# Kernel optimization log

Measured on AMD Instinct MI355X. Metric: run time of the kernel, lower is better.

Reference implementation:

```python
import jax, jax.numpy as jnp
import numpy as np

NUM_ENT = 50000
N = 4 * NUM_ENT          # concat of id/gender/age/level embeds along dim 0
D = 128                  # init_dim = gcn_dim = embed_dim
H = 4                    # k_kernel attention heads
E = 600000
NUM_REL = 10
B = 4096


def _seg_softmax(scores, seg, n):
    # scores: [E, H], softmax over edges sharing the same destination node
    m = jax.ops.segment_max(scores, seg, num_segments=n)
    m = jnp.where(jnp.isfinite(m), m, 0.0)
    e = jnp.exp(scores - m[seg])
    s = jax.ops.segment_sum(e, seg, num_segments=n)
    return e / (s[seg] + 1e-16)


def _rgat_conv(x, rel_emb, src, dst, edge_type, W, W_rel, att):
    # CompGCN-style relational message (x_src + r_et) @ W, GAT-style attention,
    # per-destination segment softmax, scatter-sum aggregate, tanh activation.
    n = x.shape[0]
    xW = x @ W                        # [N, D_out]
    rW = rel_emb @ W                  # relation embed in message space
    d_out = xW.shape[1]
    dh = d_out // H
    m = (xW[src] + rW[edge_type]).reshape(-1, H, dh)   # [E, H, dh] messages
    q = xW[dst].reshape(-1, H, dh)                     # [E, H, dh] dest feats
    score = jax.nn.leaky_relu(
        (q * att[:, :dh]).sum(-1) + (m * att[:, dh:]).sum(-1), 0.2)  # [E, H]
    alpha = _seg_softmax(score, dst, n)                # [E, H]
    out = jax.ops.segment_sum((alpha[..., None] * m).reshape(-1, d_out), dst,
                              num_segments=n)          # [N, D_out]
    return jnp.tanh(out), rel_emb @ W_rel


def setup_inputs() -> dict:
    key = jax.random.key(0)
    ks = jax.random.split(key, 16)
    s = 0.1  # weight scale for numerical sanity
    return {
        "sub": jax.random.randint(ks[0], (B,), 0, N),
        "rel": jax.random.randint(ks[1], (B,), 0, 2 * NUM_REL),
        "edge_index": jax.random.randint(ks[2], (2, E), 0, N),
        "edge_type": jax.random.randint(ks[3], (E,), 0, 2 * NUM_REL),
        "ent_feature": jax.random.randint(ks[4], (NUM_ENT, 3), 0, 8),
        "gender_weight": s * jax.random.normal(ks[5], (8, D), jnp.float32),
        "age_weight": s * jax.random.normal(ks[6], (8, D), jnp.float32),
        "level_weight": s * jax.random.normal(ks[7], (8, D), jnp.float32),
        "id_embed": s * jax.random.normal(ks[8], (NUM_ENT, D), jnp.float32),
        "init_rel": s * jax.random.normal(ks[9], (2 * NUM_REL, D), jnp.float32),
        "W1": s * jax.random.normal(ks[10], (D, D), jnp.float32),
        "Wr1": s * jax.random.normal(ks[11], (D, D), jnp.float32),
        "att1": s * jax.random.normal(ks[12], (H, 2 * (D // H)), jnp.float32),
        "W2": s * jax.random.normal(ks[13], (D, D), jnp.float32),
        "Wr2": s * jax.random.normal(ks[14], (D, D), jnp.float32),
        "att2": s * jax.random.normal(ks[15], (H, 2 * (D // H)), jnp.float32),
    }


def reference(sub, rel, edge_index, edge_type, ent_feature,
              gender_weight, age_weight, level_weight, id_embed, init_rel,
              W1, Wr1, att1, W2, Wr2, att2):
    # feature embedding gathers + concat along node axis (as in __init__)
    gender_embed = gender_weight[ent_feature[:, 0]]
    age_embed = age_weight[ent_feature[:, 1]]
    level_embed = level_weight[ent_feature[:, 2]]
    x = jnp.concatenate([id_embed, gender_embed, age_embed, level_embed], axis=0)  # [N, D]
    src, dst = edge_index[0], edge_index[1]
    r = init_rel
    x, r = _rgat_conv(x, r, src, dst, edge_type, W1, Wr1, att1)
    # dropout modules run as identity (eval mode)
    x, r = _rgat_conv(x, r, src, dst, edge_type, W2, Wr2, att2)
    sub_emb = x[sub]
    rel_emb = r[rel]
    return (sub_emb, rel_emb, x)
```

## Files before the change

kernel.cpp:

```cpp
#include <hip/hip_runtime.h>

#define D 128
#define HEADS 4

typedef __attribute__((ext_vector_type(8))) short short8;
typedef __attribute__((ext_vector_type(4))) float f32x4;

__device__ __forceinline__ short f2b(float f) {
    unsigned u = __float_as_uint(f);
    unsigned r = (u + 0x7FFFu + ((u >> 16) & 1u)) >> 16;
    return (short)r;
}

__global__ __launch_bounds__(256) void gemm_mfma(
    const unsigned short* __restrict__ Ab, const short* __restrict__ Wt,
    unsigned short* __restrict__ C, const float* __restrict__ att,
    float* __restrict__ ns, int buildmode,
    const int* __restrict__ ent_feature, const float* __restrict__ gw,
    const float* __restrict__ aw, const float* __restrict__ lw,
    const float* __restrict__ idemb, int num_ent)
{
    __shared__ short sA[64 * D];
    __shared__ short sW[D * D];

    const int t = threadIdx.x;
    const long row0 = (long)blockIdx.x * 64;

    {
        int srow = t >> 2;
        int q = t & 3;
        long grow = row0 + srow;
        if (buildmode == 2) {
            const short8* p8 = (const short8*)(Ab + grow * D);
            #pragma unroll
            for (int jb = 0; jb < 4; ++jb) {
                short8 blk = p8[q * 4 + jb];
                int kb = (q * 4 + jb) ^ (srow & 7);
                *(short8*)&sA[srow * D + kb * 8] = blk;
            }
        } else {
            const float* srcp;
            if (grow < num_ent)               srcp = idemb + grow * D;
            else if (grow < 2L * num_ent)     srcp = gw + (long)ent_feature[(grow - num_ent) * 3 + 0] * D;
            else if (grow < 3L * num_ent)     srcp = aw + (long)ent_feature[(grow - 2L * num_ent) * 3 + 1] * D;
            else                              srcp = lw + (long)ent_feature[(grow - 3L * num_ent) * 3 + 2] * D;
            const float4* p4 = (const float4*)srcp + q * 8;
            float v[32];
            #pragma unroll
            for (int j = 0; j < 8; ++j) {
                float4 f = p4[j];
                v[j * 4 + 0] = f.x; v[j * 4 + 1] = f.y; v[j * 4 + 2] = f.z; v[j * 4 + 3] = f.w;
            }
            #pragma unroll
            for (int jb = 0; jb < 4; ++jb) {
                short8 blk;
                #pragma unroll
                for (int e = 0; e < 8; ++e) blk[e] = f2b(v[jb * 8 + e]);
                int kb = (q * 4 + jb) ^ (srow & 7);
                *(short8*)&sA[srow * D + kb * 8] = blk;
            }
        }
    }

    {
        #pragma unroll
        for (int i = 0; i < 8; ++i) {
            int c = t + 256 * i;
            int row = c >> 4, kb = c & 15;
            short8 blk = *(const short8*)(Wt + c * 8);
            *(short8*)&sW[row * D + (kb ^ (row & 7)) * 8] = blk;
        }
    }
    __syncthreads();

    const int wv = t >> 6, lane = t & 63;
    const int cl = lane & 15, kg = lane >> 4;

    short8 a[4];
    #pragma unroll
    for (int ks = 0; ks < 4; ++ks)
        a[ks] = *(const short8*)&sA[(wv * 16 + cl) * D + (((ks * 4 + kg) ^ (cl & 7)) * 8)];

    f32x4 acc[8];
    #pragma unroll
    for (int ct = 0; ct < 8; ++ct) acc[ct] = (f32x4){0.f, 0.f, 0.f, 0.f};

    #pragma unroll
    for (int ct = 0; ct < 8; ++ct) {
        #pragma unroll
        for (int ks = 0; ks < 4; ++ks) {
            short8 b = *(const short8*)&sW[(ct * 16 + cl) * D + (((ks * 4 + kg) ^ (cl & 7)) * 8)];
            acc[ct] = __builtin_amdgcn_mfma_f32_16x16x32_bf16(a[ks], b, acc[ct], 0, 0, 0);
        }
    }

    unsigned short* Cp = C + (row0 + wv * 16 + kg * 4) * D;
    #pragma unroll
    for (int ct = 0; ct < 8; ++ct)
        #pragma unroll
        for (int j = 0; j < 4; ++j)
            Cp[j * D + ct * 16 + cl] = (unsigned short)f2b(acc[ct][j]);

    float aqc[8], amc[8];
    #pragma unroll
    for (int ct = 0; ct < 8; ++ct) {
        int h = ct >> 1, cc = (ct & 1) * 16 + cl;
        aqc[ct] = att[h * 64 + cc];
        amc[ct] = att[h * 64 + 32 + cc];
    }
    float* scr = (float*)sA + wv * 1024;
    #pragma unroll
    for (int pass = 0; pass < 2; ++pass) {
        __syncthreads();
        #pragma unroll
        for (int jj = 0; jj < 2; ++jj) {
            int j = pass * 2 + jj;
            f32x4 lo, hi;
            #pragma unroll
            for (int h = 0; h < 4; ++h) {
                float qv = acc[2 * h][j] * aqc[2 * h] + acc[2 * h + 1][j] * aqc[2 * h + 1];
                float sv = acc[2 * h][j] * amc[2 * h] + acc[2 * h + 1][j] * amc[2 * h + 1];
                if (h < 2) { lo[h * 2] = qv; lo[h * 2 + 1] = sv; }
                else       { hi[(h - 2) * 2] = qv; hi[(h - 2) * 2 + 1] = sv; }
            }
            int base = ((kg * 16 + cl) * 2 + jj) * 8;
            *(f32x4*)&scr[base] = lo;
            *(f32x4*)&scr[base + 4] = hi;
        }
        __syncthreads();
        int kgr = lane >> 4, rem = lane & 15;
        int jjr = rem >> 3, hr = (rem >> 1) & 3, tr = rem & 1;
        float ssum = 0.f;
        #pragma unroll
        for (int c = 0; c < 16; ++c)
            ssum += scr[((kgr * 16 + c) * 2 + jjr) * 8 + hr * 2 + tr];
        long rown = row0 + wv * 16 + kgr * 4 + pass * 2 + jjr;
        ns[rown * 8 + tr * 4 + hr] = ssum;
    }
}

__global__ void prep1(const float* __restrict__ init_rel,
                      const float* __restrict__ W1, const float* __restrict__ Wr1,
                      const float* __restrict__ W2, const float* __restrict__ att1,
                      unsigned short* __restrict__ rw16, float* __restrict__ r1,
                      float* __restrict__ srt,
                      short* __restrict__ Wt1, short* __restrict__ Wt2, int nrel)
{
    __shared__ float red[128];
    int b = blockIdx.x, c = threadIdx.x;
    if (b >= 2 * nrel) {
        int bb = b - 2 * nrel;
        const float* W = (bb < D) ? W1 : W2;
        short* Wt = (bb < D) ? Wt1 : Wt2;
        int n = bb & (D - 1);
        Wt[n * D + c] = f2b(W[c * D + n]);
        return;
    }
    int r = (b < nrel) ? b : b - nrel;
    const float* W = (b < nrel) ? W1 : Wr1;
    float s = 0.f;
    for (int k = 0; k < D; ++k) s = fmaf(init_rel[r * D + k], W[k * D + c], s);
    if (b < nrel) {
        rw16[r * D + c] = (unsigned short)f2b(s);
        int h = c >> 5;
        red[c] = s * att1[h * 64 + 32 + (c & 31)];
        __syncthreads();
        if (c < 4) {
            float ss = 0.f;
            #pragma unroll
            for (int k = 0; k < 32; ++k) ss += red[c * 32 + k];
            srt[r * 4 + c] = ss;
        }
    } else {
        r1[r * D + c] = s;
    }
}

__global__ void prep2(const float* __restrict__ r1,
                      const float* __restrict__ W2, const float* __restrict__ Wr2,
                      const float* __restrict__ att2,
                      unsigned short* __restrict__ rw16, float* __restrict__ r2,
                      float* __restrict__ srt, int nrel)
{
    __shared__ float red[128];
    int b = blockIdx.x, c = threadIdx.x;
    int r = (b < nrel) ? b : b - nrel;
    const float* W = (b < nrel) ? W2 : Wr2;
    float s = 0.f;
    for (int k = 0; k < D; ++k) s = fmaf(r1[r * D + k], W[k * D + c], s);
    if (b < nrel) {
        rw16[r * D + c] = (unsigned short)f2b(s);
        int h = c >> 5;
        red[c] = s * att2[h * 64 + 32 + (c & 31)];
        __syncthreads();
        if (c < 4) {
            float ss = 0.f;
            #pragma unroll
            for (int k = 0; k < 32; ++k) ss += red[c * 32 + k];
            srt[r * 4 + c] = ss;
        }
    } else {
        r2[r * D + c] = s;
    }
}

__global__ __launch_bounds__(256) void hist_deg(const int* __restrict__ dst,
                                                int* __restrict__ deg, int E_)
{
    int i = blockIdx.x * 256 + threadIdx.x;
    if (i < E_) atomicAdd(&deg[dst[i]], 1);
}

__global__ __launch_bounds__(256) void scan_local(const int* __restrict__ deg,
                                                  int* __restrict__ offs,
                                                  int* __restrict__ partial, int n)
{
    __shared__ int lds[256];
    int b = blockIdx.x, t = threadIdx.x;
    int base = b * 1024;
    int v[4]; int s = 0;
    #pragma unroll
    for (int j = 0; j < 4; ++j) {
        int idx = base + t * 4 + j;
        v[j] = idx < n ? deg[idx] : 0;
        s += v[j];
    }
    lds[t] = s;
    __syncthreads();
    int mysum = s;
    for (int off = 1; off < 256; off <<= 1) {
        int o = t >= off ? lds[t - off] : 0;
        __syncthreads();
        lds[t] += o;
        __syncthreads();
    }
    int excl = lds[t] - mysum;
    if (t == 255) partial[b] = lds[255];
    int run = excl;
    #pragma unroll
    for (int j = 0; j < 4; ++j) {
        int idx = base + t * 4 + j;
        if (idx < n) offs[idx] = run;
        run += v[j];
    }
}

__global__ void scan_partials(int* __restrict__ partial, int nb, int* __restrict__ offs, int n)
{
    if (threadIdx.x == 0 && blockIdx.x == 0) {
        int run = 0;
        for (int i = 0; i < nb; ++i) { int v = partial[i]; partial[i] = run; run += v; }
        offs[n] = run;
    }
}

__global__ __launch_bounds__(256) void scan_add(int* __restrict__ offs,
                                                const int* __restrict__ partial, int n)
{
    int idx = blockIdx.x * 256 + threadIdx.x;
    if (idx < n) offs[idx] += partial[idx >> 10];
}

__global__ __launch_bounds__(256) void scatter_edges(
    const int* __restrict__ src, const int* __restrict__ dst, const int* __restrict__ etype,
    const int* __restrict__ offs, int* __restrict__ deg,
    unsigned* __restrict__ sorted, int E_)
{
    int i = blockIdx.x * 256 + threadIdx.x;
    if (i >= E_) return;
    int d = dst[i];
    int pos = offs[d] + atomicSub(&deg[d], 1) - 1;
    sorted[pos] = ((unsigned)src[i] << 8) | (unsigned)etype[i];
}

#define GATHER_SLOT(mb, sv, rv, sr, p, cond)                                 \
    unsigned mb = 0, rv = 0; float sv = 0.f, sr = 0.f;                       \
    if (cond) { unsigned rowb = (p) & 0xFFFFFF00u;                           \
        unsigned etb = ((p) & 0xFFu) << 8;                                   \
        mb = *(const unsigned*)(xb + rowb + lo4);                            \
        sv = *(const float*)(nb + (rowb >> 3) + ho4);                        \
        rv = *(const unsigned*)(rb + etb + lo4);                             \
        sr = *(const float*)(sb + (etb >> 4) + (ho4 - 16)); }

#define ACCUM_SLOT(mb, sv, rv, sr, cond)                                     \
    if (cond) {                                                              \
        float mx = __uint_as_float(mb << 16) + __uint_as_float(rv << 16);    \
        float my = __uint_as_float(mb & 0xFFFF0000u) + __uint_as_float(rv & 0xFFFF0000u); \
        float sc = qd + sv + sr; sc = sc > 0.f ? sc : 0.2f * sc;             \
        float we = __expf(sc);                                               \
        srun += we; ax = fmaf(we, mx, ax); ay = fmaf(we, my, ay); }

__global__ __launch_bounds__(256) void agg_node(
    const int* __restrict__ offs, const unsigned* __restrict__ sedge,
    const unsigned short* __restrict__ xWb, const unsigned short* __restrict__ rw16,
    const float* __restrict__ ns, const float* __restrict__ srt,
    void* __restrict__ outx, int out_bf16, int Nn)
{
    int wid = threadIdx.x >> 6;
    int lane = threadIdx.x & 63;
    long node = (long)blockIdx.x * 4 + wid;
    if (node >= Nn) return;
    int h = lane >> 4;

    const char* xb = (const char*)xWb;
    const char* rb = (const char*)rw16;
    const char* nb = (const char*)ns;
    const char* sb = (const char*)srt;
    const int lo4 = 4 * lane;
    const int ho4 = 16 + 4 * h;

    float qd = ns[node * 8 + h];
    int e0 = offs[node], e1 = offs[node + 1];
    float srun = 0.f, ax = 0.f, ay = 0.f;

    for (int base = e0; base < e1; base += 4) {
        unsigned p0 = sedge[base];
        unsigned p1 = (base + 1 < e1) ? sedge[base + 1] : 0;
        unsigned p2 = (base + 2 < e1) ? sedge[base + 2] : 0;
        unsigned p3 = (base + 3 < e1) ? sedge[base + 3] : 0;

        GATHER_SLOT(m0, v0, r0, s0, p0, true)
        GATHER_SLOT(m1, v1, r1, s1, p1, base + 1 < e1)
        GATHER_SLOT(m2, v2, r2, s2, p2, base + 2 < e1)
        GATHER_SLOT(m3, v3, r3, s3, p3, base + 3 < e1)

        ACCUM_SLOT(m0, v0, r0, s0, true)
        ACCUM_SLOT(m1, v1, r1, s1, base + 1 < e1)
        ACCUM_SLOT(m2, v2, r2, s2, base + 2 < e1)
        ACCUM_SLOT(m3, v3, r3, s3, base + 3 < e1)
    }

    float inv = 1.0f / (srun + 1e-16f);
    float ox = tanhf(ax * inv);
    float oy = tanhf(ay * inv);
    if (out_bf16) {
        unsigned pk = ((unsigned)(unsigned short)f2b(oy) << 16) | (unsigned short)f2b(ox);
        *(unsigned*)((unsigned short*)outx + node * D + 2 * lane) = pk;
    } else {
        float2 o; o.x = ox; o.y = oy;
        *(float2*)((float*)outx + node * D + 2 * lane) = o;
    }
}

__global__ void gather_out(const int* __restrict__ sub, const int* __restrict__ rel,
                           const float* __restrict__ xsrc, const float* __restrict__ rsrc,
                           float* __restrict__ out_sub, float* __restrict__ out_rel, int b)
{
    long i = (long)blockIdx.x * 256 + threadIdx.x;
    long tot = (long)b * 32;
    if (i < tot) {
        long row = i >> 5; int q = (int)(i & 31);
        ((float4*)out_sub)[i] = ((const float4*)(xsrc + (long)sub[row] * D))[q];
    } else if (i < 2 * tot) {
        long j = i - tot;
        long row = j >> 5; int q = (int)(j & 31);
        ((float4*)out_rel)[j] = ((const float4*)(rsrc + (long)rel[row] * D))[q];
    }
}

extern "C" void kernel_launch(void* const* d_in, const int* in_sizes, int n_in,
                              void* d_out, int out_size, void* d_ws, size_t ws_size,
                              hipStream_t stream)
{
    const int*   sub        = (const int*)d_in[0];
    const int*   rel        = (const int*)d_in[1];
    const int*   edge_index = (const int*)d_in[2];
    const int*   edge_type  = (const int*)d_in[3];
    const int*   ent_feat   = (const int*)d_in[4];
    const float* gw         = (const float*)d_in[5];
    const float* aw         = (const float*)d_in[6];
    const float* lw         = (const float*)d_in[7];
    const float* idemb      = (const float*)d_in[8];
    const float* init_rel   = (const float*)d_in[9];
    const float* W1         = (const float*)d_in[10];
    const float* Wr1        = (const float*)d_in[11];
    const float* att1       = (const float*)d_in[12];
    const float* W2         = (const float*)d_in[13];
    const float* Wr2        = (const float*)d_in[14];
    const float* att2       = (const float*)d_in[15];

    const int  Bn      = in_sizes[0];
    const int  E_      = in_sizes[3];
    const int  num_ent = in_sizes[4] / 3;
    const long Nn      = 4L * num_ent;
    const int  nrel    = in_sizes[9] / D;

    const int* srcp = edge_index;
    const int* dstp = edge_index + E_;

    float* out_sub = (float*)d_out;
    float* out_rel = out_sub + (long)Bn * D;
    float* out_x   = out_rel + (long)Bn * D;

    unsigned short* xWb = (unsigned short*)d_ws;
    unsigned short* x1b = xWb + Nn * D;
    int*      offs   = (int*)(x1b + Nn * D);
    int*      deg    = offs + (Nn + 1);
    unsigned* sorted = (unsigned*)(deg + Nn);
    int*      partial= (int*)(sorted + E_);
    unsigned short* rw16 = (unsigned short*)(partial + 1024);
    float* r1     = (float*)(rw16 + (long)nrel * D);
    float* r2     = r1 + (long)nrel * D;
    short* Wt1    = (short*)(r2 + (long)nrel * D);
    short* Wt2    = Wt1 + D * D;
    float* ns     = (float*)(Wt2 + D * D);
    float* srt    = ns + Nn * 8;

    dim3 blk(256);
    int gemm_blocks  = (int)(Nn / 64);
    int e_blocks     = (E_ + 255) / 256;
    int agg_blocks   = (int)((Nn + 3) / 4);
    int gat_blocks   = (int)((2L * Bn * 32 + 255) / 256);
    int scan_blocks  = (int)((Nn + 1023) / 1024);
    int sadd_blocks  = (int)((Nn + 255) / 256);

    prep1<<<2 * nrel + 256, D, 0, stream>>>(init_rel, W1, Wr1, W2, att1,
                                            rw16, r1, srt, Wt1, Wt2, nrel);

    hipMemsetAsync(deg, 0, Nn * sizeof(int), stream);
    hist_deg<<<e_blocks, blk, 0, stream>>>(dstp, deg, E_);
    scan_local<<<scan_blocks, blk, 0, stream>>>(deg, offs, partial, (int)Nn);
    scan_partials<<<1, 64, 0, stream>>>(partial, scan_blocks, offs, (int)Nn);
    scan_add<<<sadd_blocks, blk, 0, stream>>>(offs, partial, (int)Nn);
    scatter_edges<<<e_blocks, blk, 0, stream>>>(srcp, dstp, edge_type, offs, deg, sorted, E_);

    gemm_mfma<<<gemm_blocks, blk, 0, stream>>>(nullptr, Wt1, xWb, att1, ns, 1,
                                               ent_feat, gw, aw, lw, idemb, num_ent);
    agg_node<<<agg_blocks, blk, 0, stream>>>(offs, sorted, xWb, rw16, ns, srt, x1b, 1, (int)Nn);

    prep2<<<2 * nrel, D, 0, stream>>>(r1, W2, Wr2, att2, rw16, r2, srt, nrel);
    gemm_mfma<<<gemm_blocks, blk, 0, stream>>>(x1b, Wt2, xWb, att2, ns, 2,
                                               nullptr, nullptr, nullptr, nullptr, nullptr, num_ent);
    agg_node<<<agg_blocks, blk, 0, stream>>>(offs, sorted, xWb, rw16, ns, srt, out_x, 0, (int)Nn);

    gather_out<<<gat_blocks, blk, 0, stream>>>(sub, rel, out_x, r2, out_sub, out_rel, Bn);
}
```

Baseline: 300.0 us.

## Reuse W tile across two row blocks, parallelize partial scan, enlarge agg blocks

The GEMM kernel now loads the transposed weight tile into LDS once and processes two 64-row sub-tiles per block, halving the number of blocks and the redundant weight loads. The single-thread serial scan over block partials becomes a 256-thread parallel LDS scan. The aggregation kernel switches to 1024-thread blocks with 16 nodes per block, and the offs buffer gets padding. The extra sub-tile loop adds syncs and may reduce GEMM parallelism, and larger agg blocks may affect occupancy.

```diff
diff --git a/kernel.cpp b/kernel.cpp
--- a/kernel.cpp
+++ b/kernel.cpp
@@ -15,7 +15,7 @@
 __global__ __launch_bounds__(256) void gemm_mfma(
     const unsigned short* __restrict__ Ab, const short* __restrict__ Wt,
     unsigned short* __restrict__ C, const float* __restrict__ att,
-    float* __restrict__ ns, int buildmode,
+    float* __restrict__ ns, int buildmode, long Mrows,
     const int* __restrict__ ent_feature, const float* __restrict__ gw,
     const float* __restrict__ aw, const float* __restrict__ lw,
     const float* __restrict__ idemb, int num_ent)
@@ -24,118 +24,121 @@
     __shared__ short sW[D * D];
 
     const int t = threadIdx.x;
-    const long row0 = (long)blockIdx.x * 64;
-
-    {
-        int srow = t >> 2;
-        int q = t & 3;
-        long grow = row0 + srow;
-        if (buildmode == 2) {
-            const short8* p8 = (const short8*)(Ab + grow * D);
-            #pragma unroll
-            for (int jb = 0; jb < 4; ++jb) {
-                short8 blk = p8[q * 4 + jb];
-                int kb = (q * 4 + jb) ^ (srow & 7);
-                *(short8*)&sA[srow * D + kb * 8] = blk;
+
+    #pragma unroll
+    for (int i = 0; i < 8; ++i) {
+        int c = t + 256 * i;
+        int row = c >> 4, kb = c & 15;
+        short8 blk = *(const short8*)(Wt + c * 8);
+        *(short8*)&sW[row * D + (kb ^ (row & 7)) * 8] = blk;
+    }
+
+    for (int sub = 0; sub < 2; ++sub) {
+        const long row0 = (long)blockIdx.x * 128 + sub * 64;
+        if (row0 >= Mrows) break;
+        if (sub) __syncthreads();
+
+        {
+            int srow = t >> 2;
+            int q = t & 3;
+            long grow = row0 + srow;
+            if (buildmode == 2) {
+                const short8* p8 = (const short8*)(Ab + grow * D);
+                #pragma unroll
+                for (int jb = 0; jb < 4; ++jb) {
+                    short8 blk = p8[q * 4 + jb];
+                    int kb = (q * 4 + jb) ^ (srow & 7);
+                    *(short8*)&sA[srow * D + kb * 8] = blk;
+                }
+            } else {
+                const float* srcp;
+                if (grow < num_ent)               srcp = idemb + grow * D;
+                else if (grow < 2L * num_ent)     srcp = gw + (long)ent_feature[(grow - num_ent) * 3 + 0] * D;
+                else if (grow < 3L * num_ent)     srcp = aw + (long)ent_feature[(grow - 2L * num_ent) * 3 + 1] * D;
+                else                              srcp = lw + (long)ent_feature[(grow - 3L * num_ent) * 3 + 2] * D;
+                const float4* p4 = (const float4*)srcp + q * 8;
+                float v[32];
+                #pragma unroll
+                for (int j = 0; j < 8; ++j) {
+                    float4 f = p4[j];
+                    v[j * 4 + 0] = f.x; v[j * 4 + 1] = f.y; v[j * 4 + 2] = f.z; v[j * 4 + 3] = f.w;
+                }
+                #pragma unroll
+                for (int jb = 0; jb < 4; ++jb) {
+                    short8 blk;
+                    #pragma unroll
+                    for (int e = 0; e < 8; ++e) blk[e] = f2b(v[jb * 8 + e]);
+                    int kb = (q * 4 + jb) ^ (srow & 7);
+                    *(short8*)&sA[srow * D + kb * 8] = blk;
+                }
             }
-        } else {
-            const float* srcp;
-            if (grow < num_ent)               srcp = idemb + grow * D;
-            else if (grow < 2L * num_ent)     srcp = gw + (long)ent_feature[(grow - num_ent) * 3 + 0] * D;
-            else if (grow < 3L * num_ent)     srcp = aw + (long)ent_feature[(grow - 2L * num_ent) * 3 + 1] * D;
-            else                              srcp = lw + (long)ent_feature[(grow - 3L * num_ent) * 3 + 2] * D;
-            const float4* p4 = (const float4*)srcp + q * 8;
-            float v[32];
-            #pragma unroll
-            for (int j = 0; j < 8; ++j) {
-                float4 f = p4[j];
-                v[j * 4 + 0] = f.x; v[j * 4 + 1] = f.y; v[j * 4 + 2] = f.z; v[j * 4 + 3] = f.w;
+        }
+        __syncthreads();
+
+        const int wv = t >> 6, lane = t & 63;
+        const int cl = lane & 15, kg = lane >> 4;
+
+        short8 a[4];
+        #pragma unroll
+        for (int ks = 0; ks < 4; ++ks)
+            a[ks] = *(const short8*)&sA[(wv * 16 + cl) * D + (((ks * 4 + kg) ^ (cl & 7)) * 8)];
+
+        f32x4 acc[8];
+        #pragma unroll
+        for (int ct = 0; ct < 8; ++ct) acc[ct] = (f32x4){0.f, 0.f, 0.f, 0.f};
+
+        #pragma unroll
+        for (int ct = 0; ct < 8; ++ct) {
+            #pragma unroll
+            for (int ks = 0; ks < 4; ++ks) {
+                short8 b = *(const short8*)&sW[(ct * 16 + cl) * D + (((ks * 4 + kg) ^ (cl & 7)) * 8)];
+                acc[ct] = __builtin_amdgcn_mfma_f32_16x16x32_bf16(a[ks], b, acc[ct], 0, 0, 0);
             }
-            #pragma unroll
-            for (int jb = 0; jb < 4; ++jb) {
-                short8 blk;
+        }
+
+        unsigned short* Cp = C + (row0 + wv * 16 + kg * 4) * D;
+        #pragma unroll
+        for (int ct = 0; ct < 8; ++ct)
+            #pragma unroll
+            for (int j = 0; j < 4; ++j)
+                Cp[j * D + ct * 16 + cl] = (unsigned short)f2b(acc[ct][j]);
+
+        float aqc[8], amc[8];
+        #pragma unroll
+        for (int ct = 0; ct < 8; ++ct) {
+            int h = ct >> 1, cc = (ct & 1) * 16 + cl;
+            aqc[ct] = att[h * 64 + cc];
+            amc[ct] = att[h * 64 + 32 + cc];
+        }
+        float* scr = (float*)sA + wv * 1024;
+        #pragma unroll
+        for (int pass = 0; pass < 2; ++pass) {
+            __syncthreads();
+            #pragma unroll
+            for (int jj = 0; jj < 2; ++jj) {
+                int j = pass * 2 + jj;
+                f32x4 lo, hi;
                 #pragma unroll
-                for (int e = 0; e < 8; ++e) blk[e] = f2b(v[jb * 8 + e]);
-                int kb = (q * 4 + jb) ^ (srow & 7);
-                *(short8*)&sA[srow * D + kb * 8] = blk;
+                for (int h = 0; h < 4; ++h) {
+                    float qv = acc[2 * h][j] * aqc[2 * h] + acc[2 * h + 1][j] * aqc[2 * h + 1];
+                    float sv = acc[2 * h][j] * amc[2 * h] + acc[2 * h + 1][j] * amc[2 * h + 1];
+                    if (h < 2) { lo[h * 2] = qv; lo[h * 2 + 1] = sv; }
+                    else       { hi[(h - 2) * 2] = qv; hi[(h - 2) * 2 + 1] = sv; }
+                }
+                int base = ((kg * 16 + cl) * 2 + jj) * 8;
+                *(f32x4*)&scr[base] = lo;
+                *(f32x4*)&scr[base + 4] = hi;
             }
-        }
-    }
-
-    {
-        #pragma unroll
-        for (int i = 0; i < 8; ++i) {
-            int c = t + 256 * i;
-            int row = c >> 4, kb = c & 15;
-            short8 blk = *(const short8*)(Wt + c * 8);
-            *(short8*)&sW[row * D + (kb ^ (row & 7)) * 8] = blk;
-        }
-    }
-    __syncthreads();
-
-    const int wv = t >> 6, lane = t & 63;
-    const int cl = lane & 15, kg = lane >> 4;
-
-    short8 a[4];
-    #pragma unroll
-    for (int ks = 0; ks < 4; ++ks)
-        a[ks] = *(const short8*)&sA[(wv * 16 + cl) * D + (((ks * 4 + kg) ^ (cl & 7)) * 8)];
-
-    f32x4 acc[8];
-    #pragma unroll
-    for (int ct = 0; ct < 8; ++ct) acc[ct] = (f32x4){0.f, 0.f, 0.f, 0.f};
-
-    #pragma unroll
-    for (int ct = 0; ct < 8; ++ct) {
-        #pragma unroll
-        for (int ks = 0; ks < 4; ++ks) {
-            short8 b = *(const short8*)&sW[(ct * 16 + cl) * D + (((ks * 4 + kg) ^ (cl & 7)) * 8)];
-            acc[ct] = __builtin_amdgcn_mfma_f32_16x16x32_bf16(a[ks], b, acc[ct], 0, 0, 0);
-        }
-    }
-
-    unsigned short* Cp = C + (row0 + wv * 16 + kg * 4) * D;
-    #pragma unroll
-    for (int ct = 0; ct < 8; ++ct)
-        #pragma unroll
-        for (int j = 0; j < 4; ++j)
-            Cp[j * D + ct * 16 + cl] = (unsigned short)f2b(acc[ct][j]);
-
-    float aqc[8], amc[8];
-    #pragma unroll
-    for (int ct = 0; ct < 8; ++ct) {
-        int h = ct >> 1, cc = (ct & 1) * 16 + cl;
-        aqc[ct] = att[h * 64 + cc];
-        amc[ct] = att[h * 64 + 32 + cc];
-    }
-    float* scr = (float*)sA + wv * 1024;
-    #pragma unroll
-    for (int pass = 0; pass < 2; ++pass) {
-        __syncthreads();
-        #pragma unroll
-        for (int jj = 0; jj < 2; ++jj) {
-            int j = pass * 2 + jj;
-            f32x4 lo, hi;
-            #pragma unroll
-            for (int h = 0; h < 4; ++h) {
-                float qv = acc[2 * h][j] * aqc[2 * h] + acc[2 * h + 1][j] * aqc[2 * h + 1];
-                float sv = acc[2 * h][j] * amc[2 * h] + acc[2 * h + 1][j] * amc[2 * h + 1];
-                if (h < 2) { lo[h * 2] = qv; lo[h * 2 + 1] = sv; }
-                else       { hi[(h - 2) * 2] = qv; hi[(h - 2) * 2 + 1] = sv; }
-            }
-            int base = ((kg * 16 + cl) * 2 + jj) * 8;
-            *(f32x4*)&scr[base] = lo;
-            *(f32x4*)&scr[base + 4] = hi;
-        }
-        __syncthreads();
-        int kgr = lane >> 4, rem = lane & 15;
-        int jjr = rem >> 3, hr = (rem >> 1) & 3, tr = rem & 1;
-        float ssum = 0.f;
-        #pragma unroll
-        for (int c = 0; c < 16; ++c)
-            ssum += scr[((kgr * 16 + c) * 2 + jjr) * 8 + hr * 2 + tr];
-        long rown = row0 + wv * 16 + kgr * 4 + pass * 2 + jjr;
-        ns[rown * 8 + tr * 4 + hr] = ssum;
+            __syncthreads();
+            int kgr = lane >> 4, rem = lane & 15;
+            int jjr = rem >> 3, hr = (rem >> 1) & 3, tr = rem & 1;
+            float ssum = 0.f;
+            #pragma unroll
+            for (int c = 0; c < 16; ++c)
+                ssum += scr[((kgr * 16 + c) * 2 + jjr) * 8 + hr * 2 + tr];
+            long rown = row0 + wv * 16 + kgr * 4 + pass * 2 + jjr;
+            ns[rown * 8 + tr * 4 + hr] = ssum;
+        }
     }
 }
 
@@ -245,13 +248,23 @@
     }
 }
 
-__global__ void scan_partials(int* __restrict__ partial, int nb, int* __restrict__ offs, int n)
-{
-    if (threadIdx.x == 0 && blockIdx.x == 0) {
-        int run = 0;
-        for (int i = 0; i < nb; ++i) { int v = partial[i]; partial[i] = run; run += v; }
-        offs[n] = run;
-    }
+__global__ void scan_partials(int* __restrict__ partial, int nb,
+                              int* __restrict__ offs, int n)
+{
+    __shared__ int lds[256];
+    int t = threadIdx.x;
+    int v = (t < nb) ? partial[t] : 0;
+    lds[t] = v;
+    __syncthreads();
+    int my = v;
+    for (int off = 1; off < 256; off <<= 1) {
+        int o = (t >= off) ? lds[t - off] : 0;
+        __syncthreads();
+        lds[t] += o;
+        __syncthreads();
+    }
+    if (t < nb) partial[t] = lds[t] - my;
+    if (t == 255) offs[n] = lds[255];
 }
 
 __global__ __launch_bounds__(256) void scan_add(int* __restrict__ offs,
@@ -290,7 +303,7 @@
         float we = __expf(sc);                                               \
         srun += we; ax = fmaf(we, mx, ax); ay = fmaf(we, my, ay); }
 
-__global__ __launch_bounds__(256) void agg_node(
+__global__ __launch_bounds__(1024) void agg_node(
     const int* __restrict__ offs, const unsigned* __restrict__ sedge,
     const unsigned short* __restrict__ xWb, const unsigned short* __restrict__ rw16,
     const float* __restrict__ ns, const float* __restrict__ srt,
@@ -298,7 +311,7 @@
 {
     int wid = threadIdx.x >> 6;
     int lane = threadIdx.x & 63;
-    long node = (long)blockIdx.x * 4 + wid;
+    long node = (long)blockIdx.x * 16 + wid;
     if (node >= Nn) return;
     int h = lane >> 4;
 
@@ -395,7 +408,7 @@
     unsigned short* xWb = (unsigned short*)d_ws;
     unsigned short* x1b = xWb + Nn * D;
     int*      offs   = (int*)(x1b + Nn * D);
-    int*      deg    = offs + (Nn + 1);
+    int*      deg    = offs + (Nn + 4);
     unsigned* sorted = (unsigned*)(deg + Nn);
     int*      partial= (int*)(sorted + E_);
     unsigned short* rw16 = (unsigned short*)(partial + 1024);
@@ -407,9 +420,9 @@
     float* srt    = ns + Nn * 8;
 
     dim3 blk(256);
-    int gemm_blocks  = (int)(Nn / 64);
+    int gemm_blocks  = (int)((Nn + 127) / 128);
     int e_blocks     = (E_ + 255) / 256;
-    int agg_blocks   = (int)((Nn + 3) / 4);
+    int agg_blocks   = (int)((Nn + 15) / 16);
     int gat_blocks   = (int)((2L * Bn * 32 + 255) / 256);
     int scan_blocks  = (int)((Nn + 1023) / 1024);
     int sadd_blocks  = (int)((Nn + 255) / 256);
@@ -420,18 +433,18 @@
     hipMemsetAsync(deg, 0, Nn * sizeof(int), stream);
     hist_deg<<<e_blocks, blk, 0, stream>>>(dstp, deg, E_);
     scan_local<<<scan_blocks, blk, 0, stream>>>(deg, offs, partial, (int)Nn);
-    scan_partials<<<1, 64, 0, stream>>>(partial, scan_blocks, offs, (int)Nn);
+    scan_partials<<<1, 256, 0, stream>>>(partial, scan_blocks, offs, (int)Nn);
     scan_add<<<sadd_blocks, blk, 0, stream>>>(offs, partial, (int)Nn);
     scatter_edges<<<e_blocks, blk, 0, stream>>>(srcp, dstp, edge_type, offs, deg, sorted, E_);
 
-    gemm_mfma<<<gemm_blocks, blk, 0, stream>>>(nullptr, Wt1, xWb, att1, ns, 1,
+    gemm_mfma<<<gemm_blocks, blk, 0, stream>>>(nullptr, Wt1, xWb, att1, ns, 1, Nn,
                                                ent_feat, gw, aw, lw, idemb, num_ent);
-    agg_node<<<agg_blocks, blk, 0, stream>>>(offs, sorted, xWb, rw16, ns, srt, x1b, 1, (int)Nn);
+    agg_node<<<agg_blocks, dim3(1024), 0, stream>>>(offs, sorted, xWb, rw16, ns, srt, x1b, 1, (int)Nn);
 
     prep2<<<2 * nrel, D, 0, stream>>>(r1, W2, Wr2, att2, rw16, r2, srt, nrel);
-    gemm_mfma<<<gemm_blocks, blk, 0, stream>>>(x1b, Wt2, xWb, att2, ns, 2,
+    gemm_mfma<<<gemm_blocks, blk, 0, stream>>>(x1b, Wt2, xWb, att2, ns, 2, Nn,
                                                nullptr, nullptr, nullptr, nullptr, nullptr, num_ent);
-    agg_node<<<agg_blocks, blk, 0, stream>>>(offs, sorted, xWb, rw16, ns, srt, out_x, 0, (int)Nn);
+    agg_node<<<agg_blocks, dim3(1024), 0, stream>>>(offs, sorted, xWb, rw16, ns, srt, out_x, 0, (int)Nn);
 
     gather_out<<<gat_blocks, blk, 0, stream>>>(sub, rel, out_x, r2, out_sub, out_rel, Bn);
 }
```

Result: slower. 308.6 us (+2.8%).
